# Optimization experiments

Measured on AMD Instinct MI355X. Metric: run time of the kernel, lower is better.

## Reference

```python
import jax, jax.numpy as jnp
import numpy as np
from jax.scipy.linalg import solve_triangular

REG = 1e-3  # DCDicL regularization hyperparameter


def _p2o(psf, H, W):
    # point-spread-function -> optical transfer function: zero-pad to (H,W),
    # circularly shift so kernel center sits at origin, then rfft2.
    ds = psf.shape[-1]
    otf = jnp.zeros(psf.shape[:-2] + (H, W), psf.dtype)
    otf = otf.at[..., :ds, :ds].set(psf)
    otf = jnp.roll(otf, (-(ds // 2), -(ds // 2)), axis=(-2, -1))
    return jnp.fft.rfft2(otf)


def _solve_fft(X, D, Y, alpha, H, W):
    # X:(N,1,Cin,H,Wf)  D:(N,Cout,Cin,H,Wf)  Y:(N,Cout,1,H,Wf)  complex64
    C_in = X.shape[2]
    a = (alpha / C_in)[..., None]              # (N,1,1,1,1) real scalar per sample
    Dc = jnp.conj(D)
    Z = Y * D + a * X                          # (N,Cout,Cin,H,Wf)
    factor1 = Z / a
    num = jnp.sum(Dc * Z, axis=2, keepdims=True)
    den = a * jnp.sum(Dc * D, axis=2, keepdims=True) + a * a  # csum: real add
    factor2 = D * (num / den)
    Xn = jnp.mean(factor1 - factor2, axis=1)   # (N,Cin,H,Wf)
    return jnp.fft.irfft2(Xn, s=(H, W))


def _solve_ls(x, d, y, alpha, reg):
    # x:(N,Cin,H,W)  d:(N,Cout,Cin,ds,ds)  y:(N,Cout,H,W)
    N, C_in, H, W = x.shape
    C_out, ds = d.shape[1], d.shape[-1]
    P = ds - 1
    M = C_in * ds * ds
    dn = ('NCHW', 'OIHW', 'NCHW')

    # All-pairs full cross-correlation (torch cal_xtx via sample-wise conv3d):
    # corr[n,i,o,u,v] = sum_{h,w} x[n,i,h+u-P,w+v-P] * x[n,o,h,w]
    def pair_corr(xn):
        return jax.lax.conv_general_dilated(xn[:, None], xn[:, None], (1, 1),
                                            [(P, P), (P, P)], dimension_numbers=dn)
    corr = jax.vmap(pair_corr)(x)              # (N, i, o, 2P+1, 2P+1)

    # Block-Toeplitz Gram (replaces unfold/flip/index-permute copies):
    # Q[n,(o,k1,k2),(i,q1,q2)] = corr[n,i,o, P+q1-k1, P+q2-k2]
    r = jnp.arange(ds)
    off = P + r[None, :] - r[:, None]          # (k, q)
    Q6 = corr[:, :, :, off[:, :, None, None], off[None, None, :, :]]  # (N,i,o,k1,q1,k2,q2)
    Q = jnp.transpose(Q6, (0, 2, 3, 5, 1, 4, 6)).reshape(N, M, M)

    # cal_xty: 'same'-padded correlation of x with y
    p = (ds - 1) // 2
    def xty_corr(xn, yn):
        return jax.lax.conv_general_dilated(xn[:, None], yn[:, None], (1, 1),
                                            [(p, p), (p, p)], dimension_numbers=dn)
    xty = jax.vmap(xty_corr)(x, y)             # (N, i, Cout, ds, ds)
    Pm = jnp.transpose(xty, (0, 1, 3, 4, 2)).reshape(N, M, C_out)

    a = (alpha * (H * W) * reg / (ds * ds * C_in)).reshape(N, 1, 1)
    Q = Q + a * jnp.eye(M, dtype=Q.dtype)
    Pm = Pm + a * jnp.transpose(d.reshape(N, C_out, M), (0, 2, 1))

    L = jnp.linalg.cholesky(Q)
    Zs = solve_triangular(L, Pm, lower=True)
    Dm = solve_triangular(jnp.swapaxes(L, -1, -2), Zs, lower=False)
    return jnp.transpose(Dm.reshape(N, C_in, ds, ds, C_out), (0, 4, 1, 2, 3))


def _forward(x, d, y, alpha_x, alpha_d, reg):
    H, W = x.shape[-2], x.shape[-1]
    X = jnp.fft.rfft2(x)[:, None]              # (N,1,Cin,H,Wf)
    D = _p2o(d, H, W)                          # (N,Cout,Cin,H,Wf)
    Y = jnp.fft.rfft2(y)[:, :, None]           # (N,Cout,1,H,Wf)
    x_new = _solve_fft(X, D, Y, alpha_x, H, W)
    d_new = _solve_ls(x_new, d, y, alpha_d, reg)
    return x_new, d_new


def setup_inputs() -> dict:
    key = jax.random.key(0)
    k0, k1, k2 = jax.random.split(key, 3)
    x = jax.random.normal(k0, (4, 64, 128, 128), jnp.float32)
    d = jax.random.normal(k1, (4, 1, 64, 5, 5), jnp.float32)
    y = jax.random.normal(k2, (4, 1, 128, 128), jnp.float32)
    alpha_x = jnp.ones((4, 1, 1, 1), jnp.float32)
    alpha_d = jnp.ones((4, 1, 1, 1), jnp.float32)
    reg = jnp.float32(REG)
    return {"x": x, "d": d, "y": y, "alpha_x": alpha_x, "alpha_d": alpha_d, "reg": reg}


def reference(x, d, y, alpha_x, alpha_d, reg):
    return _forward(x, d, y, alpha_x, alpha_d, reg)
```

## Files before the change

kernel.cpp:

```cpp
#include <hip/hip_runtime.h>
#include <hip/hip_bf16.h>
#include <math.h>

#define PI_F 3.14159265358979323846f

#define NS   4
#define CIN  64
#define HH   128
#define WW   128
#define KXN  65
#define NPIX (HH*WW)
#define MMAT 1600
#define NIT  6
#define SD   136
#define SLAB 167936

#define OFF_SINV 0
#define OFF_E    33280
#define OFF_ER   98816
#define OFF_VR   231936
#define OFF_WB   298496
#define OFF_R    364032
#define OFF_RP   1691136
#define OFF_EP   1691136
#define OFF_PP   1691136
#define OFF_XB   7196160
#define XB0C     4734976
#define OFF_DV   0
#define OFF_RV   6400
#define OFF_PV   12800
#define OFF_AP   19200
#define OFF_RV2  25600
#define OFF_PAPP 32000

#define WRED(x) { (x)+=__shfl_down((x),32); (x)+=__shfl_down((x),16); (x)+=__shfl_down((x),8); \
                  (x)+=__shfl_down((x),4);  (x)+=__shfl_down((x),2);  (x)+=__shfl_down((x),1); }

typedef __attribute__((ext_vector_type(8))) short bf16x8;
typedef __attribute__((ext_vector_type(4))) float f32x4;

__global__ __launch_bounds__(256) void k_sinv(const float* __restrict__ dict,
                                              const float* __restrict__ alpha_x,
                                              float* __restrict__ ws) {
  int idx = blockIdx.x * 256 + threadIdx.x;
  int n = blockIdx.y;
  if (idx >= HH * KXN) return;
  int ky = idx / KXN, kx = idx % KXN;
  float tr[25], ti[25];
  {
    float eyr[5], eyi[5], exr[5], exi[5];
#pragma unroll
    for (int a = 0; a < 5; ++a) {
      float s, c;
      sincosf(-2.0f * PI_F * (float)(ky * (a - 2)) / 128.0f, &s, &c);
      eyr[a] = c; eyi[a] = s;
      sincosf(-2.0f * PI_F * (float)(kx * (a - 2)) / 128.0f, &s, &c);
      exr[a] = c; exi[a] = s;
    }
#pragma unroll
    for (int a = 0; a < 5; ++a)
#pragma unroll
      for (int b = 0; b < 5; ++b) {
        tr[a*5+b] = eyr[a]*exr[b] - eyi[a]*exi[b];
        ti[a*5+b] = eyr[a]*exi[b] + eyi[a]*exr[b];
      }
  }
  const float* dn = dict + n * CIN * 25;
  float S = 0.0f;
  for (int c = 0; c < CIN; ++c) {
    const float* p = dn + c * 25;
    float Dr = 0.0f, Di = 0.0f;
#pragma unroll
    for (int t = 0; t < 25; ++t) { Dr += p[t]*tr[t]; Di += p[t]*ti[t]; }
    S += Dr*Dr + Di*Di;
  }
  float a = alpha_x[n] * (1.0f/64.0f);
  ws[OFF_SINV + (n*HH + ky)*KXN + kx] = 1.0f / (S + a);
}

__global__ __launch_bounds__(256) void k_e(const float* __restrict__ x,
                                           const float* __restrict__ dict,
                                           float* __restrict__ ws) {
  __shared__ __align__(16) float xs[68*SD];
  __shared__ float psf_s[25];
  int c = blockIdx.x, n = blockIdx.y, hh = blockIdx.z;
  int tid = threadIdx.x;
  if (tid < 25) psf_s[tid] = dict[(n*CIN + c)*25 + tid];
  const float* Xc = x + (size_t)(n*CIN + c)*NPIX;
  int rbase = hh*64 - 2;
  for (int k = tid; k < 68*132; k += 256) {
    int R = k / 132, C = k - R*132;
    int gh = (rbase + R) & 127;
    int gw = (C - 2) & 127;
    xs[R*SD + C] = Xc[gh*128 + gw];
  }
  __syncthreads();
  int cs = tid & 31, rs = tid >> 5;
  int c0 = cs*4, r0 = rs*8;
  float w[5][8];
#pragma unroll
  for (int k = 0; k < 4; ++k) {
    f32x4 a = *(const f32x4*)&xs[(r0+k)*SD + c0];
    f32x4 b = *(const f32x4*)&xs[(r0+k)*SD + c0 + 4];
#pragma unroll
    for (int e = 0; e < 4; ++e) { w[k][e] = a[e]; w[k][4+e] = b[e]; }
  }
  float* EPo = ws + OFF_EP + (size_t)(c*4 + n)*NPIX + (size_t)(hh*64 + r0)*128 + c0;
#pragma unroll
  for (int row = 0; row < 8; ++row) {
    int slot = (row + 4) % 5;
    f32x4 a = *(const f32x4*)&xs[(r0+row+4)*SD + c0];
    f32x4 b = *(const f32x4*)&xs[(r0+row+4)*SD + c0 + 4];
#pragma unroll
    for (int e = 0; e < 4; ++e) { w[slot][e] = a[e]; w[slot][4+e] = b[e]; }
    f32x4 acc = (f32x4){0.f,0.f,0.f,0.f};
#pragma unroll
    for (int u = 0; u < 5; ++u)
#pragma unroll
      for (int v = 0; v < 5; ++v) {
        float pv = psf_s[u*5 + v];
#pragma unroll
        for (int p = 0; p < 4; ++p)
          acc[p] += pv * w[(row+u) % 5][p+v];
      }
    *(f32x4*)(EPo + (size_t)row*128) = acc;
  }
}

__global__ __launch_bounds__(256) void k_e2(const float* __restrict__ y,
                                            float* __restrict__ ws) {
  int n = blockIdx.y;
  int p = blockIdx.x*256 + threadIdx.x;
  float s = 0.0f;
#pragma unroll 8
  for (int c = 0; c < CIN; ++c) s += ws[OFF_EP + (size_t)(c*4 + n)*NPIX + p];
  ws[OFF_E + n*NPIX + p] = y[n*NPIX + p] - s;
}

__global__ __launch_bounds__(256) void k_fft_rows(float* __restrict__ ws) {
  __shared__ float twr[128], twi[128];
  int tid = threadIdx.x;
  if (tid < 128) { float s, c; sincosf(-2.0f*PI_F*(float)tid/128.0f, &s, &c); twr[tid]=c; twi[tid]=s; }
  __syncthreads();
  int idx = blockIdx.x*256 + tid, n = blockIdx.y;
  if (idx >= HH*KXN) return;
  int h = idx / KXN, k = idx % KXN;
  const float* row = ws + OFF_E + (n*HH + h)*WW;
  float sr = 0, si = 0;
  for (int w = 0; w < 128; ++w) {
    int t = (w*k) & 127;
    float v = row[w];
    sr += v*twr[t]; si += v*twi[t];
  }
  float* o = ws + OFF_ER + ((n*HH + h)*KXN + k)*2;
  o[0] = sr; o[1] = si;
}

__global__ __launch_bounds__(128) void k_fft_colpipe(float* __restrict__ ws) {
  __shared__ float twr[128], twi[128];
  __shared__ float ecr[128], eci[128];
  __shared__ float ewr[128], ewi[128];
  int tid = threadIdx.x;
  int kx = blockIdx.x, n = blockIdx.y;
  { float s, c; sincosf(-2.0f*PI_F*(float)tid/128.0f, &s, &c); twr[tid]=c; twi[tid]=s; }
  const float* Er = ws + OFF_ER + (size_t)n*HH*KXN*2;
  ecr[tid] = Er[(tid*KXN + kx)*2];
  eci[tid] = Er[(tid*KXN + kx)*2 + 1];
  __syncthreads();
  {
    int ky = tid;
    float sr = 0, si = 0;
    for (int h = 0; h < 128; ++h) {
      int t = (h*ky) & 127;
      float ar = ecr[h], ai = eci[h];
      sr += ar*twr[t] - ai*twi[t];
      si += ar*twi[t] + ai*twr[t];
    }
    float sv = ws[OFF_SINV + (n*HH + ky)*KXN + kx];
    ewr[ky] = sr*sv; ewi[ky] = si*sv;
  }
  __syncthreads();
  {
    int h = tid;
    float sr = 0, si = 0;
    for (int ky = 0; ky < 128; ++ky) {
      int t = (h*ky) & 127;
      float ar = ewr[ky], ai = ewi[ky];
      sr += ar*twr[t] + ai*twi[t];
      si += ai*twr[t] - ar*twi[t];
    }
    float* o = ws + OFF_VR + ((n*HH + h)*KXN + kx)*2;
    o[0] = sr; o[1] = si;
  }
}

__global__ __launch_bounds__(256) void k_ifft_rows(float* __restrict__ ws) {
  __shared__ float twr[128], twi[128];
  int tid = threadIdx.x;
  if (tid < 128) { float s, c; sincosf(-2.0f*PI_F*(float)tid/128.0f, &s, &c); twr[tid]=c; twi[tid]=s; }
  __syncthreads();
  int idx = blockIdx.x*256 + tid, n = blockIdx.y;
  int h = idx >> 7, w = idx & 127;
  const float* Vr = ws + OFF_VR + (size_t)n*HH*KXN*2;
  float s = 0.0f;
  for (int kx = 0; kx <= 64; ++kx) {
    int t = (w*kx) & 127;
    float ar = Vr[(h*KXN + kx)*2], ai = Vr[(h*KXN + kx)*2 + 1];
    float re = ar*twr[t] + ai*twi[t];
    s += (kx == 0 || kx == 64) ? re : 2.0f*re;
  }
  ws[OFF_WB + (n*HH + h)*WW + w] = s * (1.0f/16384.0f);
}

__global__ __launch_bounds__(256) void k_xnew(const float* __restrict__ x,
                                              const float* __restrict__ dict,
                                              const float* __restrict__ ws,
                                              float* __restrict__ out) {
  __shared__ __align__(16) float xs[68*SD];
  __shared__ float psf_s[25];
  int c = blockIdx.x, n = blockIdx.y, hh = blockIdx.z;
  int tid = threadIdx.x;
  if (tid < 25) psf_s[tid] = dict[(n*CIN + c)*25 + 24 - tid];
  const float* Wb = ws + OFF_WB + (size_t)n*NPIX;
  int rbase = hh*64 - 2;
  for (int k = tid; k < 68*132; k += 256) {
    int R = k / 132, C = k - R*132;
    int gh = (rbase + R) & 127;
    int gw = (C - 2) & 127;
    xs[R*SD + C] = Wb[gh*128 + gw];
  }
  __syncthreads();
  int cs = tid & 31, rs = tid >> 5;
  int c0 = cs*4, r0 = rs*8;
  float w[5][8];
#pragma unroll
  for (int k = 0; k < 4; ++k) {
    f32x4 a = *(const f32x4*)&xs[(r0+k)*SD + c0];
    f32x4 b = *(const f32x4*)&xs[(r0+k)*SD + c0 + 4];
#pragma unroll
    for (int e = 0; e < 4; ++e) { w[k][e] = a[e]; w[k][4+e] = b[e]; }
  }
  const float* Xc = x   + (size_t)(n*CIN + c)*NPIX + (size_t)(hh*64 + r0)*128 + c0;
  float*       Oc = out + (size_t)(n*CIN + c)*NPIX + (size_t)(hh*64 + r0)*128 + c0;
#pragma unroll
  for (int row = 0; row < 8; ++row) {
    int slot = (row + 4) % 5;
    f32x4 a = *(const f32x4*)&xs[(r0+row+4)*SD + c0];
    f32x4 b = *(const f32x4*)&xs[(r0+row+4)*SD + c0 + 4];
#pragma unroll
    for (int e = 0; e < 4; ++e) { w[slot][e] = a[e]; w[slot][4+e] = b[e]; }
    f32x4 acc = *(const f32x4*)(Xc + (size_t)row*128);
#pragma unroll
    for (int u = 0; u < 5; ++u)
#pragma unroll
      for (int v = 0; v < 5; ++v) {
        float pv = psf_s[u*5 + v];
#pragma unroll
        for (int p = 0; p < 4; ++p)
          acc[p] += pv * w[(row+u) % 5][p+v];
      }
    *(f32x4*)(Oc + (size_t)row*128) = acc;
  }
}

__global__ __launch_bounds__(256) void k_pad(const float* __restrict__ xn,
                                             float* __restrict__ ws) {
  ushort* xb0 = (ushort*)(ws + OFF_XB);
  ushort* xb1 = xb0 + XB0C;
  int ch = blockIdx.y;
  int idx = blockIdx.x*256 + threadIdx.x;
  if (ch == 0 && idx == 0) xb1[0] = 0;
  if (idx >= 136*136) return;
  int hp = idx / 136, wp = idx % 136;
  float v = 0.0f;
  if (hp >= 4 && hp < 132 && wp >= 4 && wp < 132)
    v = xn[(size_t)ch*NPIX + (hp-4)*128 + (wp-4)];
  __hip_bfloat16 b = __float2bfloat16(v);
  ushort bits = *(ushort*)&b;
  size_t o = (size_t)ch*18496 + idx;
  xb0[o] = bits;
  xb1[o + 1] = bits;
}

__global__ __launch_bounds__(256, 3) void k_gemm(float* __restrict__ ws) {
  __shared__ __align__(16) ushort sA0[64*128];
  __shared__ __align__(16) ushort sA1[64*128];
  __shared__ __align__(16) ushort sB [64*128];

  const ushort* xb0 = (const ushort*)(ws + OFF_XB);
  const ushort* xb1 = xb0 + XB0C;
  int fid = blockIdx.x;
  int xcd = fid & 7, l = fid >> 3;
  int nn = xcd & 3, hi = xcd >> 2;
  int g = l % 21, m = l / 21;
  int sl = m*2 + hi;

  int tid = threadIdx.x;
  int wv = tid >> 6, lane = tid & 63;
  int l16 = lane & 15, quad = lane >> 4;
  int lr = lane >> 4, lc = lane & 15;

  int sidx0 = 2*g;
  int sidx1 = 2*g + 1;
  int sval1 = (sidx1 <= 40);
  if (sidx1 > 40) sidx1 = 40;
  int uv0 = sidx0 + 40, uv1 = sidx1 + 40;
  int u0 = uv0 / 9, v0 = uv0 % 9;
  int u1 = uv1 / 9, v1 = uv1 % 9;

  size_t chanBase = (size_t)(nn*64) * 18496;
  int ridx0 = sl * 16;
  const ushort* pB  = xb0 + chanBase + 548 + (size_t)ridx0*136;
  size_t a0e = chanBase + (size_t)(u0 + ridx0)*136 + v0;
  size_t a1e = chanBase + (size_t)(u1 + ridx0)*136 + v1;
  const ushort* pA0 = (v0 & 1) ? (xb1 + a0e + 1) : (xb0 + a0e);
  const ushort* pA1 = (v1 & 1) ? (xb1 + a1e + 1) : (xb0 + a1e);

  f32x4 acc[2][4];
#pragma unroll
  for (int s = 0; s < 2; ++s)
#pragma unroll
    for (int jt = 0; jt < 4; ++jt) acc[s][jt] = (f32x4){0.f,0.f,0.f,0.f};

  for (int r = 0; r < 16; ++r) {
    if (r) __syncthreads();
#pragma unroll
    for (int c = 0; c < 4; ++c) {
      int row = wv*16 + c*4 + lr;
      int sw = ((lc ^ (row & 15)) * 8);
      size_t goff = (size_t)row * 18496 + (size_t)lc * 8;
      {
        const uint2* p = (const uint2*)(pB + goff);
        uint2 b0 = p[0], b1 = p[1];
        *(uint2*)&sB[row*128 + sw]     = b0;
        *(uint2*)&sB[row*128 + sw + 4] = b1;
      }
      {
        const uint* p = (const uint*)(pA0 + goff);
        uint4 v4; v4.x = p[0]; v4.y = p[1]; v4.z = p[2]; v4.w = p[3];
        *(uint4*)&sA0[row*128 + sw] = v4;
      }
      {
        const uint* p = (const uint*)(pA1 + goff);
        uint4 v4; v4.x = p[0]; v4.y = p[1]; v4.z = p[2]; v4.w = p[3];
        *(uint4*)&sA1[row*128 + sw] = v4;
      }
    }
    __syncthreads();
#pragma unroll
    for (int kt = 0; kt < 4; ++kt) {
      int c16 = kt*4 + quad;
      int sw = ((c16 ^ l16) * 8);
      bf16x8 af0 = *(const bf16x8*)&sA0[(wv*16 + l16)*128 + sw];
      bf16x8 af1 = *(const bf16x8*)&sA1[(wv*16 + l16)*128 + sw];
      bf16x8 bf[4];
#pragma unroll
      for (int jt = 0; jt < 4; ++jt)
        bf[jt] = *(const bf16x8*)&sB[(jt*16 + l16)*128 + sw];
#pragma unroll
      for (int jt = 0; jt < 4; ++jt) {
        acc[0][jt] = __builtin_amdgcn_mfma_f32_16x16x32_bf16(af0, bf[jt], acc[0][jt], 0, 0, 0);
        acc[1][jt] = __builtin_amdgcn_mfma_f32_16x16x32_bf16(af1, bf[jt], acc[1][jt], 0, 0, 0);
      }
    }
    pB += 136; pA0 += 136; pA1 += 136;
  }

  int io = wv*16 + quad*4;
  {
    float* dst = ws + OFF_RP + (((size_t)nn*8 + sl)*41 + sidx0)*4096;
#pragma unroll
    for (int jt = 0; jt < 4; ++jt) {
      int jout = jt*16 + l16;
      *reinterpret_cast<f32x4*>(dst + jout*64 + io) = acc[0][jt];
    }
  }
  if (sval1) {
    float* dst = ws + OFF_RP + (((size_t)nn*8 + sl)*41 + sidx1)*4096;
#pragma unroll
    for (int jt = 0; jt < 4; ++jt) {
      int jout = jt*16 + l16;
      *reinterpret_cast<f32x4*>(dst + jout*64 + io) = acc[1][jt];
    }
  }
}

__global__ __launch_bounds__(256) void k_rsumtrans(float* __restrict__ ws) {
  __shared__ float tile[64][65];
  int s = blockIdx.x, n = blockIdx.y;
  float* base0 = ws + OFF_RP + ((size_t)n*8)*SLAB + (size_t)s*4096;
  int t = threadIdx.x;
#pragma unroll
  for (int p = 0; p < 4; ++p) {
    int vidx = p*256 + t;
    int row = vidx >> 4, c0 = (vidx & 15)*4;
    f32x4 sum = (f32x4){0.f,0.f,0.f,0.f};
#pragma unroll
    for (int sl = 0; sl < 8; ++sl)
      sum += *(const f32x4*)(base0 + (size_t)sl*SLAB + row*64 + c0);
    *(f32x4*)(base0 + row*64 + c0) = sum;
    tile[row][c0]   = sum[0]; tile[row][c0+1] = sum[1];
    tile[row][c0+2] = sum[2]; tile[row][c0+3] = sum[3];
  }
  __syncthreads();
  float* PT = base0 + SLAB;
#pragma unroll
  for (int p = 0; p < 4; ++p) {
    int vidx = p*256 + t;
    int row = vidx >> 4, c0 = (vidx & 15)*4;
    f32x4 o;
#pragma unroll
    for (int e = 0; e < 4; ++e) o[e] = tile[c0+e][row];
    *(f32x4*)(PT + row*64 + c0) = o;
  }
}

__global__ __launch_bounds__(256) void k_rmerge(float* __restrict__ ws) {
  int j = blockIdx.x, n = blockIdx.y;
  const float* P  = ws + OFF_RP + ((size_t)n*8 + 0)*SLAB;
  const float* PT = ws + OFF_RP + ((size_t)n*8 + 1)*SLAB;
  float* out = ws + OFF_R + ((size_t)(n*64 + j))*81*64;
  int t = threadIdx.x;
  for (int k = t; k < 81*64; k += 256) {
    int uv = k >> 6, i = k & 63;
    float v = (uv >= 40) ? P [(size_t)(uv-40)*4096 + j*64 + i]
                         : PT[(size_t)(40-uv)*4096 + j*64 + i];
    out[k] = v;
  }
}

__global__ __launch_bounds__(256) void k_pm(const float* __restrict__ xn,
                                            const float* __restrict__ y,
                                            float* __restrict__ ws) {
  __shared__ __align__(16) float xs[68*SD];
  __shared__ float red_s[4][25];
  int i = blockIdx.x, n = blockIdx.y, hh = blockIdx.z;
  int tid = threadIdx.x;
  const float* Xi = xn + (size_t)(n*CIN + i)*NPIX;
  int rbase = hh*64 - 2;
  for (int k = tid; k < 68*132; k += 256) {
    int R = k / 132, C = k - R*132;
    int hr = rbase + R, wc = C - 2;
    float v = 0.0f;
    if (hr >= 0 && hr < 128 && wc >= 0 && wc < 128) v = Xi[hr*128 + wc];
    xs[R*SD + C] = v;
  }
  __syncthreads();
  int cs = tid & 31, rs = tid >> 5;
  int c0 = cs*4, r0 = rs*8;
  float w[5][8];
#pragma unroll
  for (int k = 0; k < 4; ++k) {
    f32x4 a = *(const f32x4*)&xs[(r0+k)*SD + c0];
    f32x4 b = *(const f32x4*)&xs[(r0+k)*SD + c0 + 4];
#pragma unroll
    for (int e = 0; e < 4; ++e) { w[k][e] = a[e]; w[k][4+e] = b[e]; }
  }
  float acc[25];
#pragma unroll
  for (int t = 0; t < 25; ++t) acc[t] = 0.0f;
  const float* yp = y + (size_t)n*NPIX + (size_t)(hh*64 + r0)*128 + c0;
#pragma unroll
  for (int row = 0; row < 8; ++row) {
    int slot = (row + 4) % 5;
    f32x4 a = *(const f32x4*)&xs[(r0+row+4)*SD + c0];
    f32x4 b = *(const f32x4*)&xs[(r0+row+4)*SD + c0 + 4];
#pragma unroll
    for (int e = 0; e < 4; ++e) { w[slot][e] = a[e]; w[slot][4+e] = b[e]; }
    f32x4 yv = *(const f32x4*)(yp + (size_t)row*128);
#pragma unroll
    for (int u = 0; u < 5; ++u)
#pragma unroll
      for (int v = 0; v < 5; ++v) {
#pragma unroll
        for (int p = 0; p < 4; ++p)
          acc[u*5+v] += w[(row+u) % 5][p+v] * yv[p];
      }
  }
  int lane = tid & 63, wv = tid >> 6;
#pragma unroll
  for (int t = 0; t < 25; ++t) {
    float v = acc[t];
    WRED(v);
    if (lane == 0) red_s[wv][t] = v;
  }
  __syncthreads();
  if (tid < 25) {
    float s = red_s[0][tid] + red_s[1][tid] + red_s[2][tid] + red_s[3][tid];
    ws[OFF_PP + ((size_t)(hh*4 + n)*64 + i)*25 + tid] = s;
  }
}

__global__ __launch_bounds__(64) void k_pm2(const float* __restrict__ dict,
                                            const float* __restrict__ alpha_d,
                                            const float* __restrict__ regp,
                                            float* __restrict__ ws) {
  int i = blockIdx.x, n = blockIdx.y, t = threadIdx.x;
  if (t >= 25) return;
  float s = 0.0f;
#pragma unroll
  for (int tg = 0; tg < 2; ++tg) s += ws[OFF_PP + ((size_t)(tg*4 + n)*64 + i)*25 + t];
  float ad = alpha_d[n] * 16384.0f * regp[0] * (1.0f/1600.0f);
  float val = s + ad * dict[(n*CIN + i)*25 + t];
  int idx = n*MMAT + i*25 + t;
  ws[OFF_RV + idx] = val;
  ws[OFF_PV + idx] = val;
}

__global__ __launch_bounds__(256) void k_cg_first(float* __restrict__ ws,
                                                  const float* __restrict__ alpha_d,
                                                  const float* __restrict__ regp) {
  __shared__ float vv[MMAT];
  __shared__ float part[25][66];
  int n = blockIdx.y, j = blockIdx.x, tid = threadIdx.x;
  for (int t = tid; t < MMAT; t += 256) vv[t] = ws[OFF_PV + n*MMAT + t];
  __syncthreads();
  int i = tid & 63, qq = tid >> 6;
  const float* Rj = ws + OFF_R + ((size_t)(n*CIN + j))*81*64;
  const float* vi = &vv[i*25];
#pragma unroll
  for (int s6 = 0; s6 < 7; ++s6) {
    int ac = qq + 4*s6;
    if (ac < 25) {
      int a = ac/5, c = ac%5;
      float s = 0.0f;
#pragma unroll
      for (int b = 0; b < 5; ++b)
#pragma unroll
        for (int d = 0; d < 5; ++d)
          s += Rj[((4+b-a)*9 + (4+d-c))*64 + i] * vi[b*5+d];
      part[ac][i] = s;
    }
  }
  __syncthreads();
  float contrib = 0.0f;
  if (tid < 25) {
    float s = 0.0f;
    for (int t = 0; t < 64; ++t) s += part[tid][t];
    float reg = alpha_d[n] * 16384.0f * regp[0] * (1.0f/1600.0f);
    s += reg * vv[j*25 + tid];
    ws[OFF_AP + n*MMAT + j*25 + tid] = s;
    contrib = s * vv[j*25 + tid];
  }
  if (tid < 64) {
    WRED(contrib);
    if (tid == 0) ws[OFF_PAPP + 0*256 + n*64 + j] = contrib;
  }
}

__global__ __launch_bounds__(256) void k_cg_step(float* __restrict__ ws, int it,
                                                 int last, float* __restrict__ out,
                                                 const float* __restrict__ alpha_d,
                                                 const float* __restrict__ regp) {
  __shared__ float vv[MMAT];
  __shared__ float red_s[9];
  __shared__ float part[25][66];
  int n = blockIdx.y, j = blockIdx.x, tid = threadIdx.x;
  const float* rsrc = ws + ((it & 1) ? OFF_RV2 : OFF_RV) + n*MMAT;
  float*       rdst = ws + ((it & 1) ? OFF_RV  : OFF_RV2) + n*MMAT;
  int lane = tid & 63, wvi = tid >> 6;

  float rold[7], apv[7];
  float rrp = 0.0f;
#pragma unroll
  for (int t = 0; t < 7; ++t) {
    int idx = tid + 256*t;
    rold[t] = 0.0f; apv[t] = 0.0f;
    if (idx < MMAT) {
      rold[t] = rsrc[idx];
      apv[t]  = ws[OFF_AP + n*MMAT + idx];
      rrp += rold[t]*rold[t];
    }
  }
  WRED(rrp);
  if (lane == 0) red_s[wvi] = rrp;
  float pp = (tid < 64) ? ws[OFF_PAPP + it*256 + n*64 + tid] : 0.0f;
  if (tid < 64) { WRED(pp); if (tid == 0) red_s[4] = pp; }
  __syncthreads();
  float rr_old = red_s[0] + red_s[1] + red_s[2] + red_s[3];
  float alpha = rr_old / (red_s[4] + 1e-30f);

  if (last) {
    if (tid < 25) {
      int idx = n*MMAT + j*25 + tid;
      float dv = ws[OFF_DV + idx] + alpha * ws[OFF_PV + idx];
      out[4194304 + n*MMAT + j*25 + tid] = dv;
    }
    return;
  }

  float rrnp = 0.0f;
#pragma unroll
  for (int t = 0; t < 7; ++t) {
    int idx = tid + 256*t;
    if (idx < MMAT) {
      float rn = rold[t] - alpha * apv[t];
      vv[idx] = rn;
      rrnp += rn*rn;
    }
  }
  WRED(rrnp);
  __syncthreads();
  if (lane == 0) red_s[5 + wvi] = rrnp;
  __syncthreads();
  float rr_new = red_s[5] + red_s[6] + red_s[7] + red_s[8];
  float beta = rr_new / (rr_old + 1e-30f);

  int i = tid & 63, qq = tid >> 6;
  const float* Rj = ws + OFF_R + ((size_t)(n*CIN + j))*81*64;
  const float* vi = &vv[i*25];
#pragma unroll
  for (int s6 = 0; s6 < 7; ++s6) {
    int ac = qq + 4*s6;
    if (ac < 25) {
      int a = ac/5, c = ac%5;
      float s = 0.0f;
#pragma unroll
      for (int b = 0; b < 5; ++b)
#pragma unroll
        for (int d = 0; d < 5; ++d)
          s += Rj[((4+b-a)*9 + (4+d-c))*64 + i] * vi[b*5+d];
      part[ac][i] = s;
    }
  }
  __syncthreads();
  float contrib = 0.0f;
  if (tid < 25) {
    float s = 0.0f;
    for (int t = 0; t < 64; ++t) s += part[tid][t];
    float reg = alpha_d[n] * 16384.0f * regp[0] * (1.0f/1600.0f);
    float rn_seg = vv[j*25 + tid];
    s += reg * rn_seg;
    int idx = n*MMAT + j*25 + tid;
    float p_old = ws[OFF_PV + idx];
    float dv = ws[OFF_DV + idx] + alpha * p_old;
    float pn  = rn_seg + beta * p_old;
    float apn = s + beta * ws[OFF_AP + idx];
    ws[OFF_DV + idx] = dv;
    ws[OFF_PV + idx] = pn;
    ws[OFF_AP + idx] = apn;
    rdst[j*25 + tid] = rn_seg;
    contrib = pn * apn;
  }
  if (tid < 64) {
    WRED(contrib);
    if (tid == 0) ws[OFF_PAPP + (it+1)*256 + n*64 + j] = contrib;
  }
}

extern "C" void kernel_launch(void* const* d_in, const int* in_sizes, int n_in,
                              void* d_out, int out_size, void* d_ws, size_t ws_size,
                              hipStream_t stream) {
  (void)in_sizes; (void)n_in; (void)out_size; (void)ws_size;
  const float* x    = (const float*)d_in[0];
  const float* dict = (const float*)d_in[1];
  const float* y    = (const float*)d_in[2];
  const float* ax   = (const float*)d_in[3];
  const float* ad   = (const float*)d_in[4];
  const float* regp = (const float*)d_in[5];
  float* out = (float*)d_out;
  float* ws  = (float*)d_ws;

  dim3 b256(256);
  k_sinv<<<dim3(33,4), b256, 0, stream>>>(dict, ax, ws);
  k_e<<<dim3(64,4,2), b256, 0, stream>>>(x, dict, ws);
  k_e2<<<dim3(64,4), b256, 0, stream>>>(y, ws);
  k_fft_rows<<<dim3(33,4), b256, 0, stream>>>(ws);
  k_fft_colpipe<<<dim3(65,4), dim3(128), 0, stream>>>(ws);
  k_ifft_rows<<<dim3(64,4), b256, 0, stream>>>(ws);
  k_xnew<<<dim3(64,4,2), b256, 0, stream>>>(x, dict, ws, out);

  k_pad<<<dim3(73,256), b256, 0, stream>>>(out, ws);
  k_gemm<<<dim3(672), b256, 0, stream>>>(ws);
  k_rsumtrans<<<dim3(41,4), b256, 0, stream>>>(ws);
  k_rmerge<<<dim3(64,4), b256, 0, stream>>>(ws);

  k_pm<<<dim3(64,4,2), b256, 0, stream>>>(out, y, ws);
  k_pm2<<<dim3(64,4), dim3(64), 0, stream>>>(dict, ad, regp, ws);

  k_cg_first<<<dim3(64,4), b256, 0, stream>>>(ws, ad, regp);
  for (int it = 0; it < NIT; ++it)
    k_cg_step<<<dim3(64,4), b256, 0, stream>>>(ws, it, (it == NIT-1) ? 1 : 0, out, ad, regp);
}
```

Before: 272.4 us.

## Switch Gram GEMM to 32x32x16 MFMA with split-K across waves and LDS reduction

```diff
diff --git a/kernel.cpp b/kernel.cpp
--- a/kernel.cpp
+++ b/kernel.cpp
@@ -38,6 +38,7 @@
 
 typedef __attribute__((ext_vector_type(8))) short bf16x8;
 typedef __attribute__((ext_vector_type(4))) float f32x4;
+typedef __attribute__((ext_vector_type(16))) float f32x16;
 
 __global__ __launch_bounds__(256) void k_sinv(const float* __restrict__ dict,
                                               const float* __restrict__ alpha_x,
@@ -297,7 +298,8 @@
 
   int tid = threadIdx.x;
   int wv = tid >> 6, lane = tid & 63;
-  int l16 = lane & 15, quad = lane >> 4;
+  int l32 = lane & 31, half = lane >> 5;
+  int rg = wv & 1, kh = wv >> 1;
   int lr = lane >> 4, lc = lane & 15;
 
   int sidx0 = 2*g;
@@ -316,11 +318,13 @@
   const ushort* pA0 = (v0 & 1) ? (xb1 + a0e + 1) : (xb0 + a0e);
   const ushort* pA1 = (v1 & 1) ? (xb1 + a1e + 1) : (xb0 + a1e);
 
-  f32x4 acc[2][4];
+  f32x16 acc[2][2];
 #pragma unroll
   for (int s = 0; s < 2; ++s)
 #pragma unroll
-    for (int jt = 0; jt < 4; ++jt) acc[s][jt] = (f32x4){0.f,0.f,0.f,0.f};
+    for (int cg = 0; cg < 2; ++cg)
+#pragma unroll
+      for (int e = 0; e < 16; ++e) acc[s][cg][e] = 0.f;
 
   for (int r = 0; r < 16; ++r) {
     if (r) __syncthreads();
@@ -348,39 +352,61 @@
     }
     __syncthreads();
 #pragma unroll
-    for (int kt = 0; kt < 4; ++kt) {
-      int c16 = kt*4 + quad;
-      int sw = ((c16 ^ l16) * 8);
-      bf16x8 af0 = *(const bf16x8*)&sA0[(wv*16 + l16)*128 + sw];
-      bf16x8 af1 = *(const bf16x8*)&sA1[(wv*16 + l16)*128 + sw];
-      bf16x8 bf[4];
-#pragma unroll
-      for (int jt = 0; jt < 4; ++jt)
-        bf[jt] = *(const bf16x8*)&sB[(jt*16 + l16)*128 + sw];
-#pragma unroll
-      for (int jt = 0; jt < 4; ++jt) {
-        acc[0][jt] = __builtin_amdgcn_mfma_f32_16x16x32_bf16(af0, bf[jt], acc[0][jt], 0, 0, 0);
-        acc[1][jt] = __builtin_amdgcn_mfma_f32_16x16x32_bf16(af1, bf[jt], acc[1][jt], 0, 0, 0);
+    for (int ks = 0; ks < 4; ++ks) {
+      int c16 = (kh*4 + ks)*2 + half;
+      int sw = ((c16 ^ (l32 & 15)) * 8);
+      int arow = rg*32 + l32;
+      bf16x8 af0 = *(const bf16x8*)&sA0[arow*128 + sw];
+      bf16x8 af1 = *(const bf16x8*)&sA1[arow*128 + sw];
+#pragma unroll
+      for (int cg = 0; cg < 2; ++cg) {
+        int brow = cg*32 + l32;
+        bf16x8 bf = *(const bf16x8*)&sB[brow*128 + sw];
+        acc[0][cg] = __builtin_amdgcn_mfma_f32_32x32x16_bf16(af0, bf, acc[0][cg], 0, 0, 0);
+        acc[1][cg] = __builtin_amdgcn_mfma_f32_32x32x16_bf16(af1, bf, acc[1][cg], 0, 0, 0);
       }
     }
     pB += 136; pA0 += 136; pA1 += 136;
   }
 
-  int io = wv*16 + quad*4;
-  {
-    float* dst = ws + OFF_RP + (((size_t)nn*8 + sl)*41 + sidx0)*4096;
-#pragma unroll
-    for (int jt = 0; jt < 4; ++jt) {
-      int jout = jt*16 + l16;
-      *reinterpret_cast<f32x4*>(dst + jout*64 + io) = acc[0][jt];
-    }
-  }
-  if (sval1) {
-    float* dst = ws + OFF_RP + (((size_t)nn*8 + sl)*41 + sidx1)*4096;
-#pragma unroll
-    for (int jt = 0; jt < 4; ++jt) {
-      int jout = jt*16 + l16;
-      *reinterpret_cast<f32x4*>(dst + jout*64 + io) = acc[1][jt];
+  __syncthreads();
+  if (kh == 1) {
+    float* dst = (wv == 2) ? (float*)sA0 : (float*)sA1;
+#pragma unroll
+    for (int s = 0; s < 2; ++s)
+#pragma unroll
+      for (int cg = 0; cg < 2; ++cg)
+#pragma unroll
+        for (int e = 0; e < 16; ++e)
+          dst[(s*32 + cg*16 + e)*64 + lane] = acc[s][cg][e];
+  }
+  __syncthreads();
+  if (kh == 0) {
+    const float* src = (wv == 0) ? (const float*)sA0 : (const float*)sA1;
+#pragma unroll
+    for (int s = 0; s < 2; ++s)
+#pragma unroll
+      for (int cg = 0; cg < 2; ++cg)
+#pragma unroll
+        for (int e = 0; e < 16; ++e)
+          acc[s][cg][e] += src[(s*32 + cg*16 + e)*64 + lane];
+
+#pragma unroll
+    for (int s = 0; s < 2; ++s) {
+      if (s == 1 && !sval1) continue;
+      float* dst = ws + OFF_RP + (((size_t)nn*8 + sl)*41 + (s ? sidx1 : sidx0))*4096;
+#pragma unroll
+      for (int cg = 0; cg < 2; ++cg) {
+        int jout = cg*32 + l32;
+#pragma unroll
+        for (int q = 0; q < 4; ++q) {
+          int iout = rg*32 + half*4 + q*8;
+          f32x4 v;
+          v[0] = acc[s][cg][q*4+0]; v[1] = acc[s][cg][q*4+1];
+          v[2] = acc[s][cg][q*4+2]; v[3] = acc[s][cg][q*4+3];
+          *reinterpret_cast<f32x4*>(dst + jout*64 + iout) = v;
+        }
+      }
     }
   }
 }
```

Result: slower. 285.3 us (+4.7%).
